# Kernel tuning notes

Measured on AMD Instinct MI355X. Metric: run time of the kernel, lower is better.

Reference implementation:

```python
import jax, jax.numpy as jnp
import numpy as np
from jax import lax

EPS = 1e-5  # BatchNorm eps (eval mode, running stats)
HEADS = 8

# --- surrogate-gradient Heaviside (sigmoid surrogate, alpha=4) ---
@jax.custom_vjp
def spike(u):
    return (u >= 0.0).astype(u.dtype)

def _spike_fwd(u):
    return spike(u), u

def _spike_bwd(u, g):
    s = jax.nn.sigmoid(4.0 * u)
    return (g * 4.0 * s * (1.0 - s),)

spike.defvjp(_spike_fwd, _spike_bwd)

def lif(x, tau=0.5, threshold=1.0):
    """Multi-step LIF over leading time axis: v_t = tau*v_{t-1} + x_t,
    s_t = H(v_t - threshold), hard reset v_t *= (1 - s_t)."""
    def step(v, xt):
        v = tau * v + xt
        s = spike(v - threshold)
        return v * (1.0 - s), s
    _, out = lax.scan(step, jnp.zeros_like(x[0]), x)
    return out

def bn_eval(x, gamma, beta, mean, var):
    # x: (T,B,C,N); per-channel affine using running stats
    inv = gamma / jnp.sqrt(var + EPS)
    return x * inv[None, None, :, None] + (beta - mean * inv)[None, None, :, None]

def setup_inputs() -> dict:
    key = jax.random.key(0)
    ks = jax.random.split(key, 12)
    T, B, C, H, W = 4, 32, 384, 16, 16
    d = {}
    d['x'] = jax.random.normal(ks[0], (T, B, C, H, W), dtype=jnp.float32)
    # 1x1 Conv1d weights == (C_out, C_in) matrices
    sc = 1.0 / np.sqrt(C)
    d['q_w'] = jax.random.normal(ks[1], (C, C), dtype=jnp.float32) * sc
    d['q_gamma'] = jnp.ones((C,), jnp.float32)
    d['q_beta'] = jnp.zeros((C,), jnp.float32)
    d['q_mean'] = jax.random.normal(ks[2], (C,), dtype=jnp.float32) * 0.1
    d['q_var'] = jax.random.uniform(ks[3], (C,), dtype=jnp.float32) + 0.5
    d['k_w'] = jax.random.normal(ks[4], (C, C), dtype=jnp.float32) * sc
    d['k_gamma'] = jnp.ones((C,), jnp.float32)
    d['k_beta'] = jnp.zeros((C,), jnp.float32)
    d['k_mean'] = jax.random.normal(ks[5], (C,), dtype=jnp.float32) * 0.1
    d['k_var'] = jax.random.uniform(ks[6], (C,), dtype=jnp.float32) + 0.5
    d['proj_w'] = jax.random.normal(ks[7], (C, C), dtype=jnp.float32) * sc
    d['proj_b'] = jax.random.normal(ks[8], (C,), dtype=jnp.float32) * 0.01
    d['proj_gamma'] = jnp.ones((C,), jnp.float32)
    d['proj_beta'] = jnp.zeros((C,), jnp.float32)
    d['proj_mean'] = jax.random.normal(ks[9], (C,), dtype=jnp.float32) * 0.1
    d['proj_var'] = jax.random.uniform(ks[10], (C,), dtype=jnp.float32) + 0.5
    d['mem_alpha'] = jnp.float32(0.2)
    return d

def reference(x, q_w, q_gamma, q_beta, q_mean, q_var,
              k_w, k_gamma, k_beta, k_mean, k_var,
              proj_w, proj_b, proj_gamma, proj_beta, proj_mean, proj_var,
              mem_alpha):
    T, B, C, H, W = x.shape
    Hh = HEADS
    Dh = C // Hh
    N = H * W
    # proj_lif applied to raw input, then flatten spatial dims
    s = lif(x, tau=0.5, threshold=1.0).reshape(T, B, C, N)
    # q path: 1x1 conv (channel GEMM) -> BN -> LIF
    q = lif(bn_eval(jnp.einsum('tbcn,dc->tbdn', s, q_w), q_gamma, q_beta, q_mean, q_var),
            tau=0.5, threshold=1.0).reshape(T, B, Hh, Dh, N)
    # k path
    k = lif(bn_eval(jnp.einsum('tbcn,dc->tbdn', s, k_w), k_gamma, k_beta, k_mean, k_var),
            tau=0.5, threshold=1.0).reshape(T, B, Hh, Dh, N)
    # temporal decayed memory: m_0 = q_0; m_t = alpha*m_{t-1} + (1-alpha)*q_{t-1}
    def mstep(m_prev, q_prev):
        m = mem_alpha * m_prev + (1.0 - mem_alpha) * q_prev
        return m, m
    _, mems_rest = lax.scan(mstep, q[0], q[:-1])
    mems = jnp.concatenate([q[:1], mems_rest], axis=0)  # (T,B,Hh,Dh,N)
    # cat along Dh then sum == sum(mems)+sum(q)
    q_sum = jnp.sum(mems, axis=3, keepdims=True) + jnp.sum(q, axis=3, keepdims=True)
    attn = lif(q_sum, tau=0.5, threshold=0.5)  # (T,B,Hh,1,N)
    y = (attn * k).reshape(T, B, C, N)
    # proj conv (with bias) -> BN -> reshape back to (T,B,C,H,W)
    y = jnp.einsum('tbcn,dc->tbdn', y, proj_w) + proj_b[None, None, :, None]
    y = bn_eval(y, proj_gamma, proj_beta, proj_mean, proj_var)
    return y.reshape(T, B, C, H, W)
```

## Files before the change

### kernel.cpp

```cpp
#include <hip/hip_runtime.h>

#define T_ 4
#define B_ 32
#define C_ 384
#define N_ 256
#define HEADS_ 8
#define DH_ 48
#define EPS_ 1e-5f
#define NW_ (C_*C_)

typedef _Float16 f16;
typedef __attribute__((ext_vector_type(8))) _Float16 f16x8;
typedef __attribute__((ext_vector_type(16))) float f32x16;

#define PSCALE     4096.0f
#define PSCALE_INV (1.0f/4096.0f)

__global__ __launch_bounds__(256)
void prep_kernel(const float* __restrict__ x, f16* __restrict__ s,
                 const float* __restrict__ qw, const float* __restrict__ kw,
                 const float* __restrict__ pw,
                 f16* __restrict__ q2, f16* __restrict__ k2, f16* __restrict__ p2)
{
    __shared__ f16 Ls[64][72];
    if (blockIdx.z == 32) {
        int idx = (blockIdx.y * 4 + blockIdx.x) * 256 + threadIdx.x;
#pragma unroll
        for (int it = 0; it < 24; ++it) {
            {
                float w = qw[idx]; f16 a = (f16)w; f16 bb = (f16)((w - (float)a) * PSCALE);
                q2[idx] = a; q2[NW_ + idx] = bb;
            }
            {
                float w = kw[idx]; f16 a = (f16)w; f16 bb = (f16)((w - (float)a) * PSCALE);
                k2[idx] = a; k2[NW_ + idx] = bb;
            }
            {
                float w = pw[idx]; f16 a = (f16)w; f16 bb = (f16)((w - (float)a) * PSCALE);
                p2[idx] = a; p2[NW_ + idx] = bb;
            }
            idx += 6144;
        }
        return;
    }

    const int tid = threadIdx.x;
    const int n0 = blockIdx.x * 64;
    const int c0 = blockIdx.y * 64;
    const int b  = blockIdx.z;
    const int cl = tid >> 4;
    const int nl = (tid & 15) * 4;

    float v[4][4];
#pragma unroll
    for (int i = 0; i < 4; ++i)
#pragma unroll
        for (int j = 0; j < 4; ++j) v[i][j] = 0.f;

    for (int t = 0; t < T_; ++t) {
        const float* xt = x + (((size_t)t * B_ + b) * C_) * N_;
#pragma unroll
        for (int i = 0; i < 4; ++i) {
            int c = c0 + cl + 16 * i;
            float4 xv = *(const float4*)&xt[(size_t)c * N_ + n0 + nl];
            float xa[4] = {xv.x, xv.y, xv.z, xv.w};
#pragma unroll
            for (int j = 0; j < 4; ++j) {
                float vv = 0.5f * v[i][j] + xa[j];
                int sp = (vv >= 1.0f) ? 1 : 0;
                v[i][j] = sp ? 0.f : vv;
                Ls[nl + j][cl + 16 * i] = sp ? (f16)1.0f : (f16)0.0f;
            }
        }
        __syncthreads();
        {
            int r = tid >> 2, ch = (tid & 3) * 16;
            uint4 w0 = *(const uint4*)&Ls[r][ch];
            uint4 w1 = *(const uint4*)&Ls[r][ch + 8];
            f16* dst = s + (((size_t)t * B_ + b) * N_ + n0 + r) * (size_t)C_ + c0 + ch;
            *(uint4*)dst = w0;
            *(uint4*)(dst + 8) = w1;
        }
        __syncthreads();
    }
}

__global__ __launch_bounds__(256)
void qk_gemm_lif_kernel(const f16* __restrict__ Wq, const f16* __restrict__ Wk,
                        const f16* __restrict__ S,
                        const float* __restrict__ qg, const float* __restrict__ qb,
                        const float* __restrict__ qm, const float* __restrict__ qv,
                        const float* __restrict__ kg, const float* __restrict__ kb,
                        const float* __restrict__ km, const float* __restrict__ kv,
                        f16* __restrict__ q_spk, f16* __restrict__ k_spk)
{
    __shared__ __align__(16) char smem[36864];
    f16 (*As)[72]      = reinterpret_cast<f16(*)[72]>(smem);
    f16 (*Bs)[64][72]  = reinterpret_cast<f16(*)[64][72]>(smem + 18432);
    float (*P)[64]     = reinterpret_cast<float(*)[64]>(smem);

    const int tid  = threadIdx.x;
    const int lane = tid & 63;
    const int wave = tid >> 6;
    const int wm = wave & 1, wd = wave >> 1;
    const int l31 = lane & 31;
    const int lhi = lane >> 5;

    const int mb = blockIdx.x;
    const int b  = mb >> 3;
    const int n0 = (mb & 7) * 32;
    const int dp0 = blockIdx.y * 64;
    const int path = (dp0 >= C_) ? 1 : 0;
    const int d0 = dp0 - path * C_;

    const f16* W = path ? Wk : Wq;
    const float* g_  = path ? kg : qg;
    const float* be_ = path ? kb : qb;
    const float* m_  = path ? km : qm;
    const float* va_ = path ? kv : qv;
    f16* spk = path ? k_spk : q_spk;

    const int dcol = d0 + wd * 32 + l31;
    const float inv = g_[dcol] / sqrtf(va_[dcol] + EPS_);
    const float add = be_[dcol] - m_[dcol] * inv;

    const int ar = tid >> 1;
    const int ah = (tid & 1) * 32;
    const int at = ar >> 5;
    const int an = n0 + (ar & 31);
    const f16* arow = S + (((size_t)at * B_ + b) * N_ + an) * (size_t)C_;

    const int bp = tid >> 7;
    const int brr = (tid >> 1) & 63;
    const int bh = (tid & 1) * 32;
    const f16* brow = W + (size_t)bp * NW_ + (size_t)(d0 + brr) * C_;

    f32x16 acc[2][2];
#pragma unroll
    for (int ms = 0; ms < 2; ++ms)
#pragma unroll
        for (int p = 0; p < 2; ++p)
#pragma unroll
            for (int r = 0; r < 16; ++r) acc[ms][p][r] = 0.f;

    for (int kc = 0; kc < C_; kc += 64) {
        __syncthreads();
        {
            const f16* ga = arow + kc + ah;
            *(uint4*)&As[ar][ah]      = *(const uint4*)(ga);
            *(uint4*)&As[ar][ah + 8]  = *(const uint4*)(ga + 8);
            *(uint4*)&As[ar][ah + 16] = *(const uint4*)(ga + 16);
            *(uint4*)&As[ar][ah + 24] = *(const uint4*)(ga + 24);
            const f16* gb = brow + kc + bh;
            *(uint4*)&Bs[bp][brr][bh]      = *(const uint4*)(gb);
            *(uint4*)&Bs[bp][brr][bh + 8]  = *(const uint4*)(gb + 8);
            *(uint4*)&Bs[bp][brr][bh + 16] = *(const uint4*)(gb + 16);
            *(uint4*)&Bs[bp][brr][bh + 24] = *(const uint4*)(gb + 24);
        }
        __syncthreads();
#pragma unroll
        for (int kk = 0; kk < 4; ++kk) {
            const int ko = kk * 16 + lhi * 8;
            f16x8 a0 = *(const f16x8*)&As[wm * 64 + l31][ko];
            f16x8 a1 = *(const f16x8*)&As[wm * 64 + 32 + l31][ko];
            f16x8 b0 = *(const f16x8*)&Bs[0][wd * 32 + l31][ko];
            f16x8 b1 = *(const f16x8*)&Bs[1][wd * 32 + l31][ko];
            acc[0][0] = __builtin_amdgcn_mfma_f32_32x32x16_f16(a0, b0, acc[0][0], 0, 0, 0);
            acc[1][0] = __builtin_amdgcn_mfma_f32_32x32x16_f16(a1, b0, acc[1][0], 0, 0, 0);
            acc[0][1] = __builtin_amdgcn_mfma_f32_32x32x16_f16(a0, b1, acc[0][1], 0, 0, 0);
            acc[1][1] = __builtin_amdgcn_mfma_f32_32x32x16_f16(a1, b1, acc[1][1], 0, 0, 0);
        }
    }

    __syncthreads();
#pragma unroll
    for (int ms = 0; ms < 2; ++ms)
#pragma unroll
    for (int r = 0; r < 16; ++r) {
        int row = wm * 64 + ms * 32 + (r & 3) + 8 * (r >> 2) + 4 * lhi;
        float val = acc[ms][0][r] + acc[ms][1][r] * PSCALE_INV;
        P[row][wd * 32 + l31] = val * inv + add;
    }
    __syncthreads();

    {
        const int d = tid & 63;
        const int g = tid >> 6;
#pragma unroll
        for (int i = 0; i < 8; ++i) {
            const int nl = g + 4 * i;
            float v = 0.f;
#pragma unroll
            for (int t = 0; t < T_; ++t) {
                float p = P[t * 32 + nl][d];
                float vv = 0.5f * v + p;
                int sp = (vv >= 1.0f) ? 1 : 0;
                v = sp ? 0.f : vv;
                spk[(((size_t)t * B_ + b) * N_ + n0 + nl) * C_ + d0 + d] =
                    sp ? (f16)1.0f : (f16)0.0f;
            }
        }
    }
}

__global__ __launch_bounds__(256)
void head_attn_kernel(const f16* __restrict__ q_spk,
                      const float* __restrict__ alpha_p,
                      unsigned char* __restrict__ attn)
{
    int i = blockIdx.x * 256 + threadIdx.x;
    int n = i & (N_ - 1);
    int h = (i >> 8) & (HEADS_ - 1);
    int b = i >> 11;
    const float alpha = alpha_p[0];
    const int stride = B_ * HEADS_ * N_;
    float M = 0.f, v = 0.f, Sprev = 0.f;
#pragma unroll
    for (int t = 0; t < T_; ++t) {
        const uint4* p = (const uint4*)(q_spk + (((size_t)(t * B_ + b) * N_) + n) * C_ + h * DH_);
        int cnt = 0;
#pragma unroll
        for (int j = 0; j < 6; ++j) {
            uint4 w = p[j];
            cnt += __popc(w.x & 0x04000400u) + __popc(w.y & 0x04000400u)
                 + __popc(w.z & 0x04000400u) + __popc(w.w & 0x04000400u);
        }
        float Sqt = (float)cnt;
        if (t == 0) M = Sqt;
        else        M = alpha * M + (1.f - alpha) * Sprev;
        float qsum = M + Sqt;
        float vv = 0.5f * v + qsum;
        unsigned char sp = (vv >= 0.5f) ? 1 : 0;
        v = sp ? 0.f : vv;
        attn[(size_t)t * stride + i] = sp;
        Sprev = Sqt;
    }
}

__global__ __launch_bounds__(256)
void proj_gemm_kernel(const f16* __restrict__ Wp,
                      const f16* __restrict__ K,
                      const unsigned char* __restrict__ attn,
                      const float* __restrict__ bias,
                      const float* __restrict__ gamma, const float* __restrict__ beta,
                      const float* __restrict__ mean,  const float* __restrict__ var,
                      float* __restrict__ out)
{
    __shared__ __align__(16) char smem[36864];
    f16 (*As)[72]     = reinterpret_cast<f16(*)[72]>(smem);
    f16 (*Bs)[64][72] = reinterpret_cast<f16(*)[64][72]>(smem + 18432);

    const int tid  = threadIdx.x;
    const int lane = tid & 63;
    const int wave = tid >> 6;
    const int wm = wave & 1, wd = wave >> 1;
    const int l31 = lane & 31;
    const int lhi = lane >> 5;

    const int mb = blockIdx.x;
    const int tb = mb >> 1;
    const int n0 = (mb & 1) * 128;
    const int d0 = blockIdx.y * 64;

    const int dcol = d0 + wd * 32 + l31;
    const float iv = gamma[dcol] / sqrtf(var[dcol] + EPS_);
    const float ad = beta[dcol] - mean[dcol] * iv + bias[dcol] * iv;

    const int ar = tid >> 1;
    const int ah = (tid & 1) * 32;
    const int an = n0 + ar;
    const f16* arow = K + ((size_t)tb * N_ + an) * (size_t)C_;
    const unsigned char* At = attn + (size_t)tb * HEADS_ * N_;

    const int bp = tid >> 7;
    const int brr = (tid >> 1) & 63;
    const int bh = (tid & 1) * 32;
    const f16* brow = Wp + (size_t)bp * NW_ + (size_t)(d0 + brr) * C_;

    f32x16 acc[2][2];
#pragma unroll
    for (int ms = 0; ms < 2; ++ms)
#pragma unroll
        for (int p = 0; p < 2; ++p)
#pragma unroll
            for (int r = 0; r < 16; ++r) acc[ms][p][r] = 0.f;

    for (int kc = 0; kc < C_; kc += 64) {
        __syncthreads();
        {
#pragma unroll
            for (int j = 0; j < 4; ++j) {
                int c = kc + ah + 8 * j;
                int h = c / DH_;
                unsigned char am = At[(size_t)h * N_ + an];
                uint4 val = am ? *(const uint4*)(arow + c) : make_uint4(0u, 0u, 0u, 0u);
                *(uint4*)&As[ar][ah + 8 * j] = val;
            }
            const f16* gb = brow + kc + bh;
            *(uint4*)&Bs[bp][brr][bh]      = *(const uint4*)(gb);
            *(uint4*)&Bs[bp][brr][bh + 8]  = *(const uint4*)(gb + 8);
            *(uint4*)&Bs[bp][brr][bh + 16] = *(const uint4*)(gb + 16);
            *(uint4*)&Bs[bp][brr][bh + 24] = *(const uint4*)(gb + 24);
        }
        __syncthreads();
#pragma unroll
        for (int kk = 0; kk < 4; ++kk) {
            const int ko = kk * 16 + lhi * 8;
            f16x8 a0 = *(const f16x8*)&As[wm * 64 + l31][ko];
            f16x8 a1 = *(const f16x8*)&As[wm * 64 + 32 + l31][ko];
            f16x8 b0 = *(const f16x8*)&Bs[0][wd * 32 + l31][ko];
            f16x8 b1 = *(const f16x8*)&Bs[1][wd * 32 + l31][ko];
            acc[0][0] = __builtin_amdgcn_mfma_f32_32x32x16_f16(a0, b0, acc[0][0], 0, 0, 0);
            acc[1][0] = __builtin_amdgcn_mfma_f32_32x32x16_f16(a1, b0, acc[1][0], 0, 0, 0);
            acc[0][1] = __builtin_amdgcn_mfma_f32_32x32x16_f16(a0, b1, acc[0][1], 0, 0, 0);
            acc[1][1] = __builtin_amdgcn_mfma_f32_32x32x16_f16(a1, b1, acc[1][1], 0, 0, 0);
        }
    }

    float* obase = out + ((size_t)tb * C_ + dcol) * N_;
#pragma unroll
    for (int ms = 0; ms < 2; ++ms)
#pragma unroll
    for (int r = 0; r < 16; ++r) {
        int n = n0 + wm * 64 + ms * 32 + (r & 3) + 8 * (r >> 2) + 4 * lhi;
        float val = acc[ms][0][r] + acc[ms][1][r] * PSCALE_INV;
        obase[n] = val * iv + ad;
    }
}

extern "C" void kernel_launch(void* const* d_in, const int* in_sizes, int n_in,
                              void* d_out, int out_size, void* d_ws, size_t ws_size,
                              hipStream_t stream)
{
    const float* x       = (const float*)d_in[0];
    const float* q_w     = (const float*)d_in[1];
    const float* q_gamma = (const float*)d_in[2];
    const float* q_beta  = (const float*)d_in[3];
    const float* q_mean  = (const float*)d_in[4];
    const float* q_var   = (const float*)d_in[5];
    const float* k_w     = (const float*)d_in[6];
    const float* k_gamma = (const float*)d_in[7];
    const float* k_beta  = (const float*)d_in[8];
    const float* k_mean  = (const float*)d_in[9];
    const float* k_var   = (const float*)d_in[10];
    const float* proj_w  = (const float*)d_in[11];
    const float* proj_b  = (const float*)d_in[12];
    const float* p_gamma = (const float*)d_in[13];
    const float* p_beta  = (const float*)d_in[14];
    const float* p_mean  = (const float*)d_in[15];
    const float* p_var   = (const float*)d_in[16];
    const float* m_alpha = (const float*)d_in[17];

    float* out = (float*)d_out;

    const size_t SPK_BYTES = (size_t)T_ * B_ * N_ * C_ * sizeof(f16);
    const size_t W2_BYTES  = (size_t)2 * NW_ * sizeof(f16);

    unsigned char* ws = (unsigned char*)d_ws;
    size_t off = 0;
    auto carve = [&](size_t bytes) {
        off = (off + 255) & ~(size_t)255;
        void* p = ws + off;
        off += bytes;
        return p;
    };
    f16* s_f16  = (f16*)carve(SPK_BYTES);
    f16* q_spk  = (f16*)carve(SPK_BYTES);
    f16* k_spk  = (f16*)carve(SPK_BYTES);
    f16* Wq2    = (f16*)carve(W2_BYTES);
    f16* Wk2    = (f16*)carve(W2_BYTES);
    f16* Wp2    = (f16*)carve(W2_BYTES);
    unsigned char* attn = (unsigned char*)carve((size_t)T_ * B_ * HEADS_ * N_);

    dim3 pgrid1(4, 6, 33);
    prep_kernel<<<pgrid1, 256, 0, stream>>>(x, s_f16, q_w, k_w, proj_w, Wq2, Wk2, Wp2);

    dim3 qkgrid(256, 12);
    qk_gemm_lif_kernel<<<qkgrid, 256, 0, stream>>>(Wq2, Wk2, s_f16,
                                                   q_gamma, q_beta, q_mean, q_var,
                                                   k_gamma, k_beta, k_mean, k_var,
                                                   q_spk, k_spk);

    head_attn_kernel<<<(B_ * HEADS_ * N_) / 256, 256, 0, stream>>>(q_spk, m_alpha, attn);

    dim3 pjgrid(256, 6);
    proj_gemm_kernel<<<pjgrid, 256, 0, stream>>>(Wp2, k_spk, attn, proj_b,
                                                 p_gamma, p_beta, p_mean, p_var, out);
}
```

Baseline: 230.7 us.

## Replace q spike tensor with per-head atomic counts, use direct global-to-LDS loads

The q path no longer writes a full f16 spike tensor. Its GEMM epilogue ballots the spikes and atomically adds per-head popcounts into a counts buffer, which prep zeroes and head_attn reads. The GEMM tile loads switch to global_load_lds with an XOR-swizzled, unpadded LDS layout, and the prep kernel drops its LDS transpose in favour of per-thread 16-channel stores. This removes a large write and re-read of q spikes and the register staging of tiles, at the cost of atomics and uncoalesced x reads in prep.

```diff
diff --git a/kernel.cpp b/kernel.cpp
--- a/kernel.cpp
+++ b/kernel.cpp
@@ -16,15 +16,23 @@
 #define PSCALE     4096.0f
 #define PSCALE_INV (1.0f/4096.0f)
 
+typedef const __attribute__((address_space(1))) unsigned int gas_u32;
+typedef __attribute__((address_space(3))) unsigned int las_u32;
+
+__device__ __forceinline__ void gload16(const void* g, void* l) {
+    __builtin_amdgcn_global_load_lds((gas_u32*)g, (las_u32*)l, 16, 0, 0);
+}
+
 __global__ __launch_bounds__(256)
 void prep_kernel(const float* __restrict__ x, f16* __restrict__ s,
                  const float* __restrict__ qw, const float* __restrict__ kw,
                  const float* __restrict__ pw,
-                 f16* __restrict__ q2, f16* __restrict__ k2, f16* __restrict__ p2)
+                 f16* __restrict__ q2, f16* __restrict__ k2, f16* __restrict__ p2,
+                 unsigned int* __restrict__ counts)
 {
-    __shared__ f16 Ls[64][72];
     if (blockIdx.z == 32) {
-        int idx = (blockIdx.y * 4 + blockIdx.x) * 256 + threadIdx.x;
+        const int base = (blockIdx.y * 4 + blockIdx.x) * 256 + threadIdx.x;
+        int idx = base;
 #pragma unroll
         for (int it = 0; it < 24; ++it) {
             {
@@ -41,47 +49,37 @@
             }
             idx += 6144;
         }
+        const uint4 z = make_uint4(0u, 0u, 0u, 0u);
+        for (int i = base; i < (T_ * B_ * HEADS_ * N_) / 4; i += 6144)
+            ((uint4*)counts)[i] = z;
         return;
     }
 
     const int tid = threadIdx.x;
-    const int n0 = blockIdx.x * 64;
-    const int c0 = blockIdx.y * 64;
+    const int n  = blockIdx.x * 64 + (tid & 63);
+    const int cg = tid >> 6;
+    const int c0 = blockIdx.y * 64 + cg * 16;
     const int b  = blockIdx.z;
-    const int cl = tid >> 4;
-    const int nl = (tid & 15) * 4;
-
-    float v[4][4];
-#pragma unroll
-    for (int i = 0; i < 4; ++i)
-#pragma unroll
-        for (int j = 0; j < 4; ++j) v[i][j] = 0.f;
-
+
+    float v[16];
+#pragma unroll
+    for (int i = 0; i < 16; ++i) v[i] = 0.f;
+
+#pragma unroll
     for (int t = 0; t < T_; ++t) {
         const float* xt = x + (((size_t)t * B_ + b) * C_) * N_;
-#pragma unroll
-        for (int i = 0; i < 4; ++i) {
-            int c = c0 + cl + 16 * i;
-            float4 xv = *(const float4*)&xt[(size_t)c * N_ + n0 + nl];
-            float xa[4] = {xv.x, xv.y, xv.z, xv.w};
-#pragma unroll
-            for (int j = 0; j < 4; ++j) {
-                float vv = 0.5f * v[i][j] + xa[j];
-                int sp = (vv >= 1.0f) ? 1 : 0;
-                v[i][j] = sp ? 0.f : vv;
-                Ls[nl + j][cl + 16 * i] = sp ? (f16)1.0f : (f16)0.0f;
-            }
-        }
-        __syncthreads();
-        {
-            int r = tid >> 2, ch = (tid & 3) * 16;
-            uint4 w0 = *(const uint4*)&Ls[r][ch];
-            uint4 w1 = *(const uint4*)&Ls[r][ch + 8];
-            f16* dst = s + (((size_t)t * B_ + b) * N_ + n0 + r) * (size_t)C_ + c0 + ch;
-            *(uint4*)dst = w0;
-            *(uint4*)(dst + 8) = w1;
-        }
-        __syncthreads();
+        union { f16 h[16]; uint4 q[2]; } u;
+#pragma unroll
+        for (int i = 0; i < 16; ++i) {
+            float xv = xt[(size_t)(c0 + i) * N_ + n];
+            float vv = 0.5f * v[i] + xv;
+            int sp = (vv >= 1.0f) ? 1 : 0;
+            v[i] = sp ? 0.f : vv;
+            u.h[i] = sp ? (f16)1.0f : (f16)0.0f;
+        }
+        f16* dst = s + (((size_t)t * B_ + b) * N_ + n) * (size_t)C_ + c0;
+        *(uint4*)dst = u.q[0];
+        *(uint4*)(dst + 8) = u.q[1];
     }
 }
 
@@ -92,12 +90,12 @@
                         const float* __restrict__ qm, const float* __restrict__ qv,
                         const float* __restrict__ kg, const float* __restrict__ kb,
                         const float* __restrict__ km, const float* __restrict__ kv,
-                        f16* __restrict__ q_spk, f16* __restrict__ k_spk)
+                        unsigned int* __restrict__ counts, f16* __restrict__ k_spk)
 {
-    __shared__ __align__(16) char smem[36864];
-    f16 (*As)[72]      = reinterpret_cast<f16(*)[72]>(smem);
-    f16 (*Bs)[64][72]  = reinterpret_cast<f16(*)[64][72]>(smem + 18432);
-    float (*P)[64]     = reinterpret_cast<float(*)[64]>(smem);
+    __shared__ __align__(16) char smem[32768];
+    f16* ldsA = (f16*)smem;
+    f16* ldsB = ldsA + 128 * 64;
+    float (*P)[64] = reinterpret_cast<float(*)[64]>(smem);
 
     const int tid  = threadIdx.x;
     const int lane = tid & 63;
@@ -105,6 +103,7 @@
     const int wm = wave & 1, wd = wave >> 1;
     const int l31 = lane & 31;
     const int lhi = lane >> 5;
+    const int lr = lane >> 3, lc = lane & 7;
 
     const int mb = blockIdx.x;
     const int b  = mb >> 3;
@@ -118,22 +117,23 @@
     const float* be_ = path ? kb : qb;
     const float* m_  = path ? km : qm;
     const float* va_ = path ? kv : qv;
-    f16* spk = path ? k_spk : q_spk;
 
     const int dcol = d0 + wd * 32 + l31;
     const float inv = g_[dcol] / sqrtf(va_[dcol] + EPS_);
     const float add = be_[dcol] - m_[dcol] * inv;
 
-    const int ar = tid >> 1;
-    const int ah = (tid & 1) * 32;
-    const int at = ar >> 5;
-    const int an = n0 + (ar & 31);
-    const f16* arow = S + (((size_t)at * B_ + b) * N_ + an) * (size_t)C_;
-
-    const int bp = tid >> 7;
-    const int brr = (tid >> 1) & 63;
-    const int bh = (tid & 1) * 32;
-    const f16* brow = W + (size_t)bp * NW_ + (size_t)(d0 + brr) * C_;
+    const f16* gA[4]; const f16* gB[4];
+    f16* dA[4]; f16* dB[4];
+#pragma unroll
+    for (int j = 0; j < 4; ++j) {
+        const int rr = wave * 32 + j * 8 + lr;
+        const int t = rr >> 5, n = n0 + (rr & 31);
+        gA[j] = S + (((size_t)t * B_ + b) * N_ + n) * (size_t)C_ + (lc ^ lr) * 8;
+        const int p = rr >> 6, r = rr & 63;
+        gB[j] = W + (size_t)p * NW_ + (size_t)(d0 + r) * C_ + (lc ^ lr) * 8;
+        dA[j] = ldsA + (wave * 32 + j * 8) * 64;
+        dB[j] = ldsB + (wave * 32 + j * 8) * 64;
+    }
 
     f32x16 acc[2][2];
 #pragma unroll
@@ -142,29 +142,28 @@
         for (int p = 0; p < 2; ++p)
 #pragma unroll
             for (int r = 0; r < 16; ++r) acc[ms][p][r] = 0.f;
+
+    const f16* pa0 = ldsA + (wm * 64 + l31) * 64;
+    const f16* pa1 = pa0 + 32 * 64;
+    const f16* pb0 = ldsB + (wd * 32 + l31) * 64;
+    const f16* pb1 = pb0 + 64 * 64;
+    const int sx = l31 & 7;
 
     for (int kc = 0; kc < C_; kc += 64) {
         __syncthreads();
-        {
-            const f16* ga = arow + kc + ah;
-            *(uint4*)&As[ar][ah]      = *(const uint4*)(ga);
-            *(uint4*)&As[ar][ah + 8]  = *(const uint4*)(ga + 8);
-            *(uint4*)&As[ar][ah + 16] = *(const uint4*)(ga + 16);
-            *(uint4*)&As[ar][ah + 24] = *(const uint4*)(ga + 24);
-            const f16* gb = brow + kc + bh;
-            *(uint4*)&Bs[bp][brr][bh]      = *(const uint4*)(gb);
-            *(uint4*)&Bs[bp][brr][bh + 8]  = *(const uint4*)(gb + 8);
-            *(uint4*)&Bs[bp][brr][bh + 16] = *(const uint4*)(gb + 16);
-            *(uint4*)&Bs[bp][brr][bh + 24] = *(const uint4*)(gb + 24);
+#pragma unroll
+        for (int j = 0; j < 4; ++j) {
+            gload16(gA[j] + kc, dA[j]);
+            gload16(gB[j] + kc, dB[j]);
         }
         __syncthreads();
 #pragma unroll
         for (int kk = 0; kk < 4; ++kk) {
-            const int ko = kk * 16 + lhi * 8;
-            f16x8 a0 = *(const f16x8*)&As[wm * 64 + l31][ko];
-            f16x8 a1 = *(const f16x8*)&As[wm * 64 + 32 + l31][ko];
-            f16x8 b0 = *(const f16x8*)&Bs[0][wd * 32 + l31][ko];
-            f16x8 b1 = *(const f16x8*)&Bs[1][wd * 32 + l31][ko];
+            const int co = ((kk * 2 + lhi) ^ sx) * 8;
+            f16x8 a0 = *(const f16x8*)(pa0 + co);
+            f16x8 a1 = *(const f16x8*)(pa1 + co);
+            f16x8 b0 = *(const f16x8*)(pb0 + co);
+            f16x8 b1 = *(const f16x8*)(pb1 + co);
             acc[0][0] = __builtin_amdgcn_mfma_f32_32x32x16_f16(a0, b0, acc[0][0], 0, 0, 0);
             acc[1][0] = __builtin_amdgcn_mfma_f32_32x32x16_f16(a1, b0, acc[1][0], 0, 0, 0);
             acc[0][1] = __builtin_amdgcn_mfma_f32_32x32x16_f16(a0, b1, acc[0][1], 0, 0, 0);
@@ -177,8 +176,8 @@
     for (int ms = 0; ms < 2; ++ms)
 #pragma unroll
     for (int r = 0; r < 16; ++r) {
-        int row = wm * 64 + ms * 32 + (r & 3) + 8 * (r >> 2) + 4 * lhi;
-        float val = acc[ms][0][r] + acc[ms][1][r] * PSCALE_INV;
+        const int row = wm * 64 + ms * 32 + (r & 3) + 8 * (r >> 2) + 4 * lhi;
+        const float val = acc[ms][0][r] + acc[ms][1][r] * PSCALE_INV;
         P[row][wd * 32 + l31] = val * inv + add;
     }
     __syncthreads();
@@ -186,46 +185,61 @@
     {
         const int d = tid & 63;
         const int g = tid >> 6;
-#pragma unroll
-        for (int i = 0; i < 8; ++i) {
-            const int nl = g + 4 * i;
-            float v = 0.f;
-#pragma unroll
-            for (int t = 0; t < T_; ++t) {
-                float p = P[t * 32 + nl][d];
-                float vv = 0.5f * v + p;
-                int sp = (vv >= 1.0f) ? 1 : 0;
-                v = sp ? 0.f : vv;
-                spk[(((size_t)t * B_ + b) * N_ + n0 + nl) * C_ + d0 + d] =
-                    sp ? (f16)1.0f : (f16)0.0f;
+        if (path == 0) {
+            const int h0 = d0 / DH_;
+            const int ls = (h0 + 1) * DH_ - d0;
+            const unsigned long long lom = (1ull << ls) - 1ull;
+#pragma unroll
+            for (int i = 0; i < 8; ++i) {
+                const int nl = g + 4 * i;
+                float v = 0.f;
+#pragma unroll
+                for (int t = 0; t < T_; ++t) {
+                    float p = P[t * 32 + nl][d];
+                    float vv = 0.5f * v + p;
+                    int sp = (vv >= 1.0f) ? 1 : 0;
+                    v = sp ? 0.f : vv;
+                    unsigned long long m = __ballot(sp);
+                    if (lane == 0) {
+                        const int base = ((t * B_ + b) * HEADS_) * N_ + n0 + nl;
+                        atomicAdd(&counts[base + h0 * N_],
+                                  (unsigned int)__popcll(m & lom));
+                        atomicAdd(&counts[base + (h0 + 1) * N_],
+                                  (unsigned int)__popcll(m & ~lom));
+                    }
+                }
             }
+        } else {
+#pragma unroll
+            for (int i = 0; i < 8; ++i) {
+                const int nl = g + 4 * i;
+                float v = 0.f;
+#pragma unroll
+                for (int t = 0; t < T_; ++t) {
+                    float p = P[t * 32 + nl][d];
+                    float vv = 0.5f * v + p;
+                    int sp = (vv >= 1.0f) ? 1 : 0;
+                    v = sp ? 0.f : vv;
+                    k_spk[(((size_t)t * B_ + b) * N_ + n0 + nl) * C_ + d0 + d] =
+                        sp ? (f16)1.0f : (f16)0.0f;
+                }
+            }
         }
     }
 }
 
 __global__ __launch_bounds__(256)
-void head_attn_kernel(const f16* __restrict__ q_spk,
+void head_attn_kernel(const unsigned int* __restrict__ counts,
                       const float* __restrict__ alpha_p,
                       unsigned char* __restrict__ attn)
 {
-    int i = blockIdx.x * 256 + threadIdx.x;
-    int n = i & (N_ - 1);
-    int h = (i >> 8) & (HEADS_ - 1);
-    int b = i >> 11;
+    const int i = blockIdx.x * 256 + threadIdx.x;
     const float alpha = alpha_p[0];
     const int stride = B_ * HEADS_ * N_;
     float M = 0.f, v = 0.f, Sprev = 0.f;
 #pragma unroll
     for (int t = 0; t < T_; ++t) {
-        const uint4* p = (const uint4*)(q_spk + (((size_t)(t * B_ + b) * N_) + n) * C_ + h * DH_);
-        int cnt = 0;
-#pragma unroll
-        for (int j = 0; j < 6; ++j) {
-            uint4 w = p[j];
-            cnt += __popc(w.x & 0x04000400u) + __popc(w.y & 0x04000400u)
-                 + __popc(w.z & 0x04000400u) + __popc(w.w & 0x04000400u);
-        }
-        float Sqt = (float)cnt;
+        float Sqt = (float)counts[t * stride + i];
         if (t == 0) M = Sqt;
         else        M = alpha * M + (1.f - alpha) * Sprev;
         float qsum = M + Sqt;
@@ -246,9 +260,9 @@
                       const float* __restrict__ mean,  const float* __restrict__ var,
                       float* __restrict__ out)
 {
-    __shared__ __align__(16) char smem[36864];
-    f16 (*As)[72]     = reinterpret_cast<f16(*)[72]>(smem);
-    f16 (*Bs)[64][72] = reinterpret_cast<f16(*)[64][72]>(smem + 18432);
+    __shared__ __align__(16) char smem[32768];
+    f16* ldsA = (f16*)smem;
+    f16* ldsB = ldsA + 128 * 64;
 
     const int tid  = threadIdx.x;
     const int lane = tid & 63;
@@ -256,6 +270,7 @@
     const int wm = wave & 1, wd = wave >> 1;
     const int l31 = lane & 31;
     const int lhi = lane >> 5;
+    const int lr = lane >> 3, lc = lane & 7;
 
     const int mb = blockIdx.x;
     const int tb = mb >> 1;
@@ -266,16 +281,20 @@
     const float iv = gamma[dcol] / sqrtf(var[dcol] + EPS_);
     const float ad = beta[dcol] - mean[dcol] * iv + bias[dcol] * iv;
 
-    const int ar = tid >> 1;
-    const int ah = (tid & 1) * 32;
-    const int an = n0 + ar;
+    const int ar  = tid >> 1;
+    const int ach = (tid & 1) * 4;
+    const int an  = n0 + ar;
     const f16* arow = K + ((size_t)tb * N_ + an) * (size_t)C_;
     const unsigned char* At = attn + (size_t)tb * HEADS_ * N_;
 
-    const int bp = tid >> 7;
-    const int brr = (tid >> 1) & 63;
-    const int bh = (tid & 1) * 32;
-    const f16* brow = Wp + (size_t)bp * NW_ + (size_t)(d0 + brr) * C_;
+    const f16* gB[4]; f16* dB[4];
+#pragma unroll
+    for (int j = 0; j < 4; ++j) {
+        const int rr = wave * 32 + j * 8 + lr;
+        const int p = rr >> 6, r = rr & 63;
+        gB[j] = Wp + (size_t)p * NW_ + (size_t)(d0 + r) * C_ + (lc ^ lr) * 8;
+        dB[j] = ldsB + (wave * 32 + j * 8) * 64;
+    }
 
     f32x16 acc[2][2];
 #pragma unroll
@@ -284,32 +303,34 @@
         for (int p = 0; p < 2; ++p)
 #pragma unroll
             for (int r = 0; r < 16; ++r) acc[ms][p][r] = 0.f;
+
+    const f16* pa0 = ldsA + (wm * 64 + l31) * 64;
+    const f16* pa1 = pa0 + 32 * 64;
+    const f16* pb0 = ldsB + (wd * 32 + l31) * 64;
+    const f16* pb1 = pb0 + 64 * 64;
+    const int sx = l31 & 7;
 
     for (int kc = 0; kc < C_; kc += 64) {
         __syncthreads();
-        {
-#pragma unroll
-            for (int j = 0; j < 4; ++j) {
-                int c = kc + ah + 8 * j;
-                int h = c / DH_;
-                unsigned char am = At[(size_t)h * N_ + an];
-                uint4 val = am ? *(const uint4*)(arow + c) : make_uint4(0u, 0u, 0u, 0u);
-                *(uint4*)&As[ar][ah + 8 * j] = val;
-            }
-            const f16* gb = brow + kc + bh;
-            *(uint4*)&Bs[bp][brr][bh]      = *(const uint4*)(gb);
-            *(uint4*)&Bs[bp][brr][bh + 8]  = *(const uint4*)(gb + 8);
-            *(uint4*)&Bs[bp][brr][bh + 16] = *(const uint4*)(gb + 16);
-            *(uint4*)&Bs[bp][brr][bh + 24] = *(const uint4*)(gb + 24);
+#pragma unroll
+        for (int j = 0; j < 4; ++j) gload16(gB[j] + kc, dB[j]);
+#pragma unroll
+        for (int j = 0; j < 4; ++j) {
+            const int c8 = ach + j;
+            const int c = kc + c8 * 8;
+            const int h = c / DH_;
+            const unsigned char am = At[(size_t)h * N_ + an];
+            uint4 val = am ? *(const uint4*)(arow + c) : make_uint4(0u, 0u, 0u, 0u);
+            *(uint4*)(ldsA + ar * 64 + ((c8 ^ (ar & 7)) * 8)) = val;
         }
         __syncthreads();
 #pragma unroll
         for (int kk = 0; kk < 4; ++kk) {
-            const int ko = kk * 16 + lhi * 8;
-            f16x8 a0 = *(const f16x8*)&As[wm * 64 + l31][ko];
-            f16x8 a1 = *(const f16x8*)&As[wm * 64 + 32 + l31][ko];
-            f16x8 b0 = *(const f16x8*)&Bs[0][wd * 32 + l31][ko];
-            f16x8 b1 = *(const f16x8*)&Bs[1][wd * 32 + l31][ko];
+            const int co = ((kk * 2 + lhi) ^ sx) * 8;
+            f16x8 a0 = *(const f16x8*)(pa0 + co);
+            f16x8 a1 = *(const f16x8*)(pa1 + co);
+            f16x8 b0 = *(const f16x8*)(pb0 + co);
+            f16x8 b1 = *(const f16x8*)(pb1 + co);
             acc[0][0] = __builtin_amdgcn_mfma_f32_32x32x16_f16(a0, b0, acc[0][0], 0, 0, 0);
             acc[1][0] = __builtin_amdgcn_mfma_f32_32x32x16_f16(a1, b0, acc[1][0], 0, 0, 0);
             acc[0][1] = __builtin_amdgcn_mfma_f32_32x32x16_f16(a0, b1, acc[0][1], 0, 0, 0);
@@ -322,8 +343,8 @@
     for (int ms = 0; ms < 2; ++ms)
 #pragma unroll
     for (int r = 0; r < 16; ++r) {
-        int n = n0 + wm * 64 + ms * 32 + (r & 3) + 8 * (r >> 2) + 4 * lhi;
-        float val = acc[ms][0][r] + acc[ms][1][r] * PSCALE_INV;
+        const int n = n0 + wm * 64 + ms * 32 + (r & 3) + 8 * (r >> 2) + 4 * lhi;
+        const float val = acc[ms][0][r] + acc[ms][1][r] * PSCALE_INV;
         obase[n] = val * iv + ad;
     }
 }
@@ -355,6 +376,7 @@
 
     const size_t SPK_BYTES = (size_t)T_ * B_ * N_ * C_ * sizeof(f16);
     const size_t W2_BYTES  = (size_t)2 * NW_ * sizeof(f16);
+    const size_t TBHN      = (size_t)T_ * B_ * HEADS_ * N_;
 
     unsigned char* ws = (unsigned char*)d_ws;
     size_t off = 0;
@@ -365,23 +387,24 @@
         return p;
     };
     f16* s_f16  = (f16*)carve(SPK_BYTES);
-    f16* q_spk  = (f16*)carve(SPK_BYTES);
     f16* k_spk  = (f16*)carve(SPK_BYTES);
     f16* Wq2    = (f16*)carve(W2_BYTES);
     f16* Wk2    = (f16*)carve(W2_BYTES);
     f16* Wp2    = (f16*)carve(W2_BYTES);
-    unsigned char* attn = (unsigned char*)carve((size_t)T_ * B_ * HEADS_ * N_);
+    unsigned char* attn   = (unsigned char*)carve(TBHN);
+    unsigned int*  counts = (unsigned int*)carve(TBHN * 4);
 
     dim3 pgrid1(4, 6, 33);
-    prep_kernel<<<pgrid1, 256, 0, stream>>>(x, s_f16, q_w, k_w, proj_w, Wq2, Wk2, Wp2);
+    prep_kernel<<<pgrid1, 256, 0, stream>>>(x, s_f16, q_w, k_w, proj_w,
+                                            Wq2, Wk2, Wp2, counts);
 
     dim3 qkgrid(256, 12);
     qk_gemm_lif_kernel<<<qkgrid, 256, 0, stream>>>(Wq2, Wk2, s_f16,
                                                    q_gamma, q_beta, q_mean, q_var,
                                                    k_gamma, k_beta, k_mean, k_var,
-                                                   q_spk, k_spk);
-
-    head_attn_kernel<<<(B_ * HEADS_ * N_) / 256, 256, 0, stream>>>(q_spk, m_alpha, attn);
+                                                   counts, k_spk);
+
+    head_attn_kernel<<<(B_ * HEADS_ * N_) / 256, 256, 0, stream>>>(counts, m_alpha, attn);
 
     dim3 pjgrid(256, 6);
     proj_gemm_kernel<<<pjgrid, 256, 0, stream>>>(Wp2, k_spk, attn, proj_b,
```

New measurement: 241.6 us. 1.05x slower.
